# Kernel tuning notes

Measured on AMD Instinct MI355X. Metric: run time of the kernel, lower is better.

The kernel has to match this reference:

```python
import jax, jax.numpy as jnp
import numpy as np

EPS = 1e-5

def _layernorm(x, gamma, beta):
    # normalize over last (channel) axis, per point
    mu = jnp.mean(x, axis=-1, keepdims=True)
    var = jnp.mean(jnp.square(x - mu), axis=-1, keepdims=True)
    return (x - mu) * jax.lax.rsqrt(var + EPS) * gamma + beta

def setup_inputs() -> dict:
    key = jax.random.key(0)
    ks = jax.random.split(key, 12)
    B, N, C, F = 32, 4096, 3, 1024
    points = jax.random.normal(ks[0], (B, N, C), dtype=jnp.float32)
    mask = jax.random.randint(ks[1], (B, 1, N), 0, 2, dtype=jnp.int32)
    s = 0.05
    return {
        "points": points,
        "mask": mask,
        "w1": jax.random.normal(ks[2], (128, C), dtype=jnp.float32) * s,      # conv1 (no bias)
        "g1": jnp.ones((128,), jnp.float32),                                   # norm1 gamma
        "be1": jnp.zeros((128,), jnp.float32),                                 # norm1 beta
        "w2": jax.random.normal(ks[3], (256, 128), dtype=jnp.float32) * s,     # conv2
        "b2": jax.random.normal(ks[4], (256,), dtype=jnp.float32) * s,
        "w3": jax.random.normal(ks[5], (512, 512), dtype=jnp.float32) * s,     # conv3 (no bias)
        "g2": jnp.ones((512,), jnp.float32),                                   # norm2 gamma
        "be2": jnp.zeros((512,), jnp.float32),                                 # norm2 beta
        "w4": jax.random.normal(ks[6], (F, 512), dtype=jnp.float32) * s,       # conv4
        "b4": jax.random.normal(ks[7], (F,), dtype=jnp.float32) * s,
    }

def reference(points, mask, w1, g1, be1, w2, b2, w3, g2, be2, w4, b4):
    # points: [B, N, C]; mask: [B, 1, N]
    vis = (mask[:, 0, :] != 0).astype(points.dtype)[..., None]  # [B, N, 1]
    # conv1 (1x1, no bias) as point-wise matmul
    h0 = jnp.einsum('bnc,kc->bnk', points, w1)                  # [B, N, 128]
    # masked LayerNorm: LN is per-point over channels, so compute densely and zero invisible points
    h1 = _layernorm(h0, g1, be1) * vis
    h2 = jax.nn.relu(h1)
    h3 = jnp.einsum('bnk,ok->bno', h2, w2) + b2                 # [B, N, 256]
    gmax = jnp.max(h3, axis=1, keepdims=True)                   # [B, 1, 256]
    dist = jnp.concatenate([jnp.broadcast_to(gmax, h3.shape), h3], axis=-1)  # [B, N, 512]
    h4 = jnp.einsum('bno,po->bnp', dist, w3)                    # [B, N, 512]
    h5 = _layernorm(h4, g2, be2) * vis
    h6 = jax.nn.relu(h5)
    h7 = jnp.einsum('bnp,fp->bnf', h6, w4) + b4                 # [B, N, F]
    return jnp.max(h7, axis=1)                                  # [B, F]
```

## Files before the change

kernel.cpp:

```cpp
#include <hip/hip_runtime.h>
#include <stdint.h>

#define LN_EPS 1e-5f

static __device__ __forceinline__ unsigned short f2bf_bits(float f) {
  union { float f; unsigned u; } v; v.f = f;
  unsigned r = v.u + 0x7FFFu + ((v.u >> 16) & 1u);
  return (unsigned short)(r >> 16);
}
static __device__ __forceinline__ float bf2f(unsigned short h) {
  union { unsigned u; float f; } v; v.u = ((unsigned)h) << 16;
  return v.f;
}

typedef __bf16 bf16x8 __attribute__((ext_vector_type(8)));
typedef float floatx4 __attribute__((ext_vector_type(4)));

typedef __attribute__((address_space(1))) unsigned int* gas_ptr;
typedef __attribute__((address_space(3))) unsigned int* las_ptr;
static __device__ __forceinline__ void async_cp16(const void* g, void* l) {
  __builtin_amdgcn_global_load_lds((gas_ptr)g, (las_ptr)l, 16, 0, 0);
}

__global__ __launch_bounds__(256) void perm_kernel(
    const int* __restrict__ mask, int* __restrict__ newrow, int* __restrict__ cnt) {
  const int b = blockIdx.x, t = threadIdx.x;
  const int base = b * 4096 + t * 16;
  int v[16]; int s = 0;
#pragma unroll
  for (int i = 0; i < 16; ++i) { v[i] = (mask[base + i] != 0); s += v[i]; }
  const int lane = t & 63, wv = t >> 6;
  int scan = s;
  for (int o = 1; o < 64; o <<= 1) { int x = __shfl_up(scan, o); if (lane >= o) scan += x; }
  __shared__ int wsum[4], woff[4], stotal;
  if (lane == 63) wsum[wv] = scan;
  __syncthreads();
  if (t == 0) { int a = 0; for (int k = 0; k < 4; ++k) { woff[k] = a; a += wsum[k]; } stotal = a; cnt[b] = a; }
  __syncthreads();
  const int excl = scan - s + woff[wv];
  const int total = stotal;
  int run = 0;
#pragma unroll
  for (int i = 0; i < 16; ++i) {
    const int pos = t * 16 + i;
    const int visBefore = excl + run;
    newrow[b * 4096 + pos] = v[i] ? visBefore : total + (pos - visBefore);
    run += v[i];
  }
}

__global__ __launch_bounds__(256) void conv1_ln_kernel(
    const float* __restrict__ points,
    const float* __restrict__ w1, const float* __restrict__ g1,
    const float* __restrict__ be1, unsigned short* __restrict__ h2,
    const int* __restrict__ newrow, const int* __restrict__ cnt,
    const float* __restrict__ w2, const float* __restrict__ b2,
    const float* __restrict__ w3, const float* __restrict__ w4,
    unsigned short* __restrict__ w2b, unsigned short* __restrict__ w4b,
    unsigned short* __restrict__ w23b, float* __restrict__ vecb,
    int* __restrict__ hdr, unsigned short* __restrict__ tl128,
    unsigned short* __restrict__ tl256) {
  if (blockIdx.x >= 32768) {
    const int bb = blockIdx.x - 32768;
    if (bb < 2176) {
      int idx = bb * 256 + threadIdx.x;
      if (idx < 32768) w2b[idx] = f2bf_bits(w2[idx]);
      else w4b[idx - 32768] = f2bf_bits(w4[idx - 32768]);
    } else if (bb < 2176 + 256) {
      const int tid = threadIdx.x;
      const int p = (bb - 2176) * 2 + (tid >> 7);
      const int c = tid & 127;
      const float* w3r = w3 + (size_t)p * 512 + 256;
      float s = 0.f;
      for (int k = 0; k < 256; ++k) s += w3r[k] * w2[k * 128 + c];
      w23b[p * 128 + c] = f2bf_bits(s);
      if (c == 0) {
        float vb = 0.f;
        for (int k = 0; k < 256; ++k) vb += w3r[k] * b2[k];
        vecb[p] = vb;
      }
    } else {
      const int lane = threadIdx.x;
      if (lane < 64) {
        const int c = (lane < 32) ? cnt[lane] : 0;
        const int n128 = (c + 127) >> 7;
        const int n256 = (c + 255) >> 8;
        int s128 = n128, s256 = n256;
        for (int o = 1; o < 64; o <<= 1) {
          int x = __shfl_up(s128, o); if (lane >= o) s128 += x;
          int y = __shfl_up(s256, o); if (lane >= o) s256 += y;
        }
        if (lane == 31) { hdr[0] = s128; hdr[1] = s256; }
        if (lane < 32) {
          const int e128 = s128 - n128, e256 = s256 - n256;
          for (int j = 0; j < n128; ++j) tl128[e128 + j] = (unsigned short)(lane * 32 + j);
          for (int j = 0; j < n256; ++j) tl256[e256 + j] = (unsigned short)(lane * 16 + j);
        }
      }
    }
    return;
  }
  const int lane = threadIdx.x & 63;
  const int wv = threadIdx.x >> 6;
  const size_t p = (size_t)blockIdx.x * 4 + wv;
  const int dest = newrow[p];
  const int cntb = cnt[p >> 12];
  const int ceilv = (cntb + 127) & ~127;
  if (dest >= ceilv) return;
  const bool vis = (dest < cntb);
  const float x0 = points[p * 3 + 0];
  const float x1 = points[p * 3 + 1];
  const float x2 = points[p * 3 + 2];
  const int c0 = lane * 2, c1 = c0 + 1;
  float h00 = w1[c0 * 3] * x0 + w1[c0 * 3 + 1] * x1 + w1[c0 * 3 + 2] * x2;
  float h01 = w1[c1 * 3] * x0 + w1[c1 * 3 + 1] * x1 + w1[c1 * 3 + 2] * x2;
  float s = h00 + h01;
  for (int o = 32; o; o >>= 1) s += __shfl_xor(s, o);
  const float mu = s * (1.f / 128.f);
  const float d0 = h00 - mu, d1 = h01 - mu;
  float q = d0 * d0 + d1 * d1;
  for (int o = 32; o; o >>= 1) q += __shfl_xor(q, o);
  const float rs = rsqrtf(q * (1.f / 128.f) + LN_EPS);
  const float y0 = vis ? fmaxf(d0 * rs * g1[c0] + be1[c0], 0.f) : 0.f;
  const float y1 = vis ? fmaxf(d1 * rs * g1[c1] + be1[c1], 0.f) : 0.f;
  union { unsigned u; unsigned short s2[2]; } pk;
  pk.s2[0] = f2bf_bits(y0);
  pk.s2[1] = f2bf_bits(y1);
  const size_t prow = (p & ~(size_t)4095) + (size_t)dest;
  ((unsigned*)h2)[prow * 64 + lane] = pk.u;
}

__global__ __launch_bounds__(256) void gemm23_fused(
    const unsigned short* __restrict__ A,
    const unsigned short* __restrict__ w2b, const unsigned short* __restrict__ w23b,
    unsigned short* __restrict__ h46, float* __restrict__ pg,
    const float* __restrict__ b2, const float* __restrict__ vecb,
    const int* __restrict__ hdr, const unsigned short* __restrict__ tl128) {
  __shared__ __align__(16) char smA[2][128 * 64];
  __shared__ __align__(16) char smB[2][128 * 64];
  __shared__ float lmax[2][128];

  const int nW = hdr[0] * 6;
  const int cw = (nW + 7) >> 3;
  const int slot = blockIdx.x >> 3;
  const int wI = (blockIdx.x & 7) * cw + slot;
  if (slot >= cw || wI >= nW) return;
  const int t6 = wI / 6;
  const int colTile = wI - t6 * 6;
  const int rowTile = tl128[t6];

  const int tid = threadIdx.x;
  const int lane = tid & 63;
  const int w = tid >> 6;
  const int wm = w >> 1, wn = w & 1;

  const bool isPG = (colTile < 2);
  const int colBase = isPG ? colTile * 128 : (colTile - 2) * 128;
  const size_t rowBase = (size_t)rowTile * 128;
  const unsigned short* Bw = isPG ? w2b : w23b;

  floatx4 acc[4][4];
  const floatx4 zero = {0.f, 0.f, 0.f, 0.f};
#pragma unroll
  for (int i = 0; i < 4; ++i)
#pragma unroll
    for (int j = 0; j < 4; ++j) acc[i][j] = zero;

  const int rSub = lane >> 2;
  const int cb16 = (lane & 3) * 16;
  const size_t Kb = 256;
  const char* gA = (const char*)A + (rowBase + (size_t)(w * 32 + rSub)) * Kb + cb16;
  const char* gB = (const char*)Bw + ((size_t)colBase + (size_t)(w * 32 + rSub)) * Kb + cb16;
  char* lA0 = smA[0] + w * 2048;
  char* lA1 = smA[1] + w * 2048;
  char* lB0 = smB[0] + w * 2048;
  char* lB1 = smB[1] + w * 2048;
  const size_t skip16 = 16 * Kb;

  const int fm = lane & 15, fq = lane >> 4;
  const int fOff = fm * 64 + fq * 16;
  const char* pa0 = smA[0] + wm * 64 * 64 + fOff;
  const char* pa1 = smA[1] + wm * 64 * 64 + fOff;
  const char* pb0 = smB[0] + wn * 64 * 64 + fOff;
  const char* pb1 = smB[1] + wn * 64 * 64 + fOff;

  for (int k0 = 0; k0 < 128; k0 += 64) {
    async_cp16(gA, lA0);
    async_cp16(gA + skip16, lA0 + 1024);
    async_cp16(gA + 64, lA1);
    async_cp16(gA + 64 + skip16, lA1 + 1024);
    async_cp16(gB, lB0);
    async_cp16(gB + skip16, lB0 + 1024);
    async_cp16(gB + 64, lB1);
    async_cp16(gB + 64 + skip16, lB1 + 1024);
    gA += 128; gB += 128;
    __syncthreads();
    bf16x8 af0[4], bg0[4], af1[4], bg1[4];
#pragma unroll
    for (int i = 0; i < 4; ++i) af0[i] = *(const bf16x8*)(pa0 + i * 16 * 64);
#pragma unroll
    for (int j = 0; j < 4; ++j) bg0[j] = *(const bf16x8*)(pb0 + j * 16 * 64);
#pragma unroll
    for (int i = 0; i < 4; ++i)
#pragma unroll
      for (int j = 0; j < 4; ++j)
        acc[i][j] = __builtin_amdgcn_mfma_f32_16x16x32_bf16(af0[i], bg0[j], acc[i][j], 0, 0, 0);
#pragma unroll
    for (int i = 0; i < 4; ++i) af1[i] = *(const bf16x8*)(pa1 + i * 16 * 64);
#pragma unroll
    for (int j = 0; j < 4; ++j) bg1[j] = *(const bf16x8*)(pb1 + j * 16 * 64);
#pragma unroll
    for (int i = 0; i < 4; ++i)
#pragma unroll
      for (int j = 0; j < 4; ++j)
        acc[i][j] = __builtin_amdgcn_mfma_f32_16x16x32_bf16(af1[i], bg1[j], acc[i][j], 0, 0, 0);
    __syncthreads();
  }

  if (isPG) {
    float m4[4] = {-1e30f, -1e30f, -1e30f, -1e30f};
#pragma unroll
    for (int j = 0; j < 4; ++j) {
      const float ex = b2[colBase + wn * 64 + j * 16 + fm];
#pragma unroll
      for (int i = 0; i < 4; ++i)
#pragma unroll
        for (int r = 0; r < 4; ++r) m4[j] = fmaxf(m4[j], acc[i][j][r] + ex);
      m4[j] = fmaxf(m4[j], __shfl_xor(m4[j], 16));
      m4[j] = fmaxf(m4[j], __shfl_xor(m4[j], 32));
    }
    const float sel = (fq == 0) ? m4[0] : (fq == 1) ? m4[1] : (fq == 2) ? m4[2] : m4[3];
    lmax[wm][wn * 64 + fq * 16 + fm] = sel;
    __syncthreads();
    if (tid < 128) {
      const float v = fmaxf(lmax[0][tid], lmax[1][tid]);
      pg[(size_t)rowTile * 256 + colBase + tid] = v;
    }
  } else {
#pragma unroll
    for (int j = 0; j < 4; ++j) {
      const int col = colBase + wn * 64 + j * 16 + fm;
      const float ex = vecb[col];
#pragma unroll
      for (int i = 0; i < 4; ++i) {
        const size_t row0 = rowBase + wm * 64 + i * 16 + fq * 4;
#pragma unroll
        for (int r = 0; r < 4; ++r) {
          h46[(row0 + r) * 512 + col] = f2bf_bits(acc[i][j][r] + ex);
        }
      }
    }
  }
}

#define G4_BAR() __builtin_amdgcn_s_barrier()
#define G4_LGKM0() asm volatile("s_waitcnt lgkmcnt(0)" ::: "memory")
#define G4_LGKM8() asm volatile("s_waitcnt lgkmcnt(8)" ::: "memory")
#define G4_VM2() asm volatile("s_waitcnt vmcnt(2)" ::: "memory")
#define G4_VM0() asm volatile("s_waitcnt vmcnt(0)" ::: "memory")
#define G4_PRIO1() __builtin_amdgcn_s_setprio(1)
#define G4_PRIO0() __builtin_amdgcn_s_setprio(0)

#define G4_STG(bufi, h4, kt) do { \
  const char* _s = (((h4) < 2) ? srcA : srcB) + (size_t)((h4) & 1) * (128 * 1024) + (size_t)(kt) * 128; \
  char* _d = stDst + (bufi) * 65536 + ((h4) >> 1) * 32768 + ((h4) & 1) * 16384; \
  async_cp16(_s, _d); \
  async_cp16(_s + 64 * 1024, _d + 8192); \
} while (0)

#define G4_LDA(bufi, mh) do { \
  const char* _p = rdA + (bufi) * 65536 + (mh) * 8192; \
  af[0][0] = *(const bf16x8*)(_p + c0);        af[0][1] = *(const bf16x8*)(_p + c1); \
  af[1][0] = *(const bf16x8*)(_p + 2048 + c0); af[1][1] = *(const bf16x8*)(_p + 2048 + c1); \
  af[2][0] = *(const bf16x8*)(_p + 4096 + c0); af[2][1] = *(const bf16x8*)(_p + 4096 + c1); \
  af[3][0] = *(const bf16x8*)(_p + 6144 + c0); af[3][1] = *(const bf16x8*)(_p + 6144 + c1); \
} while (0)

#define G4_LDB(bufi, nh, bgx) do { \
  const char* _p = rdB + (bufi) * 65536 + (nh) * 4096; \
  bgx[0][0] = *(const bf16x8*)(_p + c0);        bgx[0][1] = *(const bf16x8*)(_p + c1); \
  bgx[1][0] = *(const bf16x8*)(_p + 2048 + c0); bgx[1][1] = *(const bf16x8*)(_p + 2048 + c1); \
} while (0)

#define G4_QUAD(mh, nh, bgx) do { \
  _Pragma("unroll") \
  for (int _m = 0; _m < 4; ++_m) { \
    _Pragma("unroll") \
    for (int _n = 0; _n < 2; ++_n) { \
      acc[(mh) * 4 + _m][(nh) * 2 + _n] = __builtin_amdgcn_mfma_f32_16x16x32_bf16( \
          af[_m][0], bgx[_n][0], acc[(mh) * 4 + _m][(nh) * 2 + _n], 0, 0, 0); \
      acc[(mh) * 4 + _m][(nh) * 2 + _n] = __builtin_amdgcn_mfma_f32_16x16x32_bf16( \
          af[_m][1], bgx[_n][1], acc[(mh) * 4 + _m][(nh) * 2 + _n], 0, 0, 0); \
    } \
  } \
} while (0)

__global__ __launch_bounds__(512, 2) void gemm4_8ph(
    const unsigned short* __restrict__ A, const unsigned short* __restrict__ Bw,
    float* __restrict__ outp2, const int* __restrict__ hdr,
    const unsigned short* __restrict__ tl256) {
  extern __shared__ char sm[];

  const int nW = hdr[1] * 4;
  const int cw = (nW + 7) >> 3;
  const int slot = blockIdx.x >> 3;
  const int wI = (blockIdx.x & 7) * cw + slot;
  if (slot >= cw || wI >= nW) return;
  const int rowTile = tl256[wI >> 2];
  const int colTile = wI & 3;

  const int tid = threadIdx.x;
  const int lane = tid & 63;
  const int w = tid >> 6;
  const int wm = w >> 2, wn = w & 3;

  const size_t rowBase = (size_t)rowTile * 256;
  const int colBase = colTile * 256;

  const int rr = tid >> 3;
  const int csw = ((tid & 7) ^ (rr & 7)) << 4;
  const char* srcA = (const char*)A + (rowBase + (size_t)rr) * 1024 + csw;
  const char* srcB = (const char*)Bw + ((size_t)colBase + (size_t)rr) * 1024 + csw;
  char* stDst = sm + w * 1024;

  const int fr = lane & 15, fq = lane >> 4;
  const int c0 = (fq * 16) ^ ((lane & 7) << 4);
  const int c1 = ((fq * 16) | 64) ^ ((lane & 7) << 4);
  const char* rdA = sm + (wm * 128 + fr) * 128;
  const char* rdB = sm + 32768 + (wn * 64 + fr) * 128;

  floatx4 acc[8][4];
  const floatx4 zero = {0.f, 0.f, 0.f, 0.f};
#pragma unroll
  for (int i = 0; i < 8; ++i)
#pragma unroll
    for (int j = 0; j < 4; ++j) acc[i][j] = zero;

  bf16x8 af[4][2], bg0[2][2], bg1[2][2];

  G4_STG(0, 0, 0); G4_STG(0, 1, 0); G4_STG(0, 2, 0); G4_STG(0, 3, 0);
  G4_STG(1, 0, 1);
  G4_VM2(); G4_BAR();

  for (int it = 0; it < 3; ++it) {
    const int tO = 2 * it + 1, tE2 = 2 * it + 2, tO2 = 2 * it + 3;
    G4_LDA(0, 0); G4_LDB(0, 0, bg0); G4_STG(1, 1, tO); G4_LGKM8(); G4_BAR(); G4_LGKM0();
    G4_PRIO1(); G4_QUAD(0, 0, bg0); G4_PRIO0(); G4_BAR();
    G4_LDB(0, 1, bg1); G4_STG(1, 2, tO); G4_BAR(); G4_LGKM0();
    G4_PRIO1(); G4_QUAD(0, 1, bg1); G4_PRIO0(); G4_BAR();
    G4_LDA(0, 1); G4_STG(1, 3, tO); G4_BAR(); G4_LGKM0();
    G4_PRIO1(); G4_QUAD(1, 1, bg1); G4_PRIO0(); G4_BAR();
    G4_STG(0, 0, tE2); G4_VM2(); G4_BAR();
    G4_PRIO1(); G4_QUAD(1, 0, bg0); G4_PRIO0(); G4_BAR();
    G4_LDA(1, 0); G4_LDB(1, 0, bg0); G4_STG(0, 1, tE2); G4_LGKM8(); G4_BAR(); G4_LGKM0();
    G4_PRIO1(); G4_QUAD(0, 0, bg0); G4_PRIO0(); G4_BAR();
    G4_LDB(1, 1, bg1); G4_STG(0, 2, tE2); G4_BAR(); G4_LGKM0();
    G4_PRIO1(); G4_QUAD(0, 1, bg1); G4_PRIO0(); G4_BAR();
    G4_LDA(1, 1); G4_STG(0, 3, tE2); G4_BAR(); G4_LGKM0();
    G4_PRIO1(); G4_QUAD(1, 1, bg1); G4_PRIO0(); G4_BAR();
    G4_STG(1, 0, tO2); G4_VM2(); G4_BAR();
    G4_PRIO1(); G4_QUAD(1, 0, bg0); G4_PRIO0(); G4_BAR();
  }

  G4_LDA(0, 0); G4_LDB(0, 0, bg0); G4_STG(1, 1, 7); G4_LGKM8(); G4_BAR(); G4_LGKM0();
  G4_PRIO1(); G4_QUAD(0, 0, bg0); G4_PRIO0(); G4_BAR();
  G4_LDB(0, 1, bg1); G4_STG(1, 2, 7); G4_BAR(); G4_LGKM0();
  G4_PRIO1(); G4_QUAD(0, 1, bg1); G4_PRIO0(); G4_BAR();
  G4_LDA(0, 1); G4_STG(1, 3, 7); G4_BAR(); G4_LGKM0();
  G4_PRIO1(); G4_QUAD(1, 1, bg1); G4_PRIO0(); G4_BAR();
  G4_VM0(); G4_BAR();
  G4_PRIO1(); G4_QUAD(1, 0, bg0); G4_PRIO0(); G4_BAR();
  G4_LDA(1, 0); G4_LDB(1, 0, bg0); G4_BAR(); G4_LGKM0();
  G4_PRIO1(); G4_QUAD(0, 0, bg0); G4_PRIO0(); G4_BAR();
  G4_LDB(1, 1, bg1); G4_BAR(); G4_LGKM0();
  G4_PRIO1(); G4_QUAD(0, 1, bg1); G4_PRIO0(); G4_BAR();
  G4_LDA(1, 1); G4_BAR(); G4_LGKM0();
  G4_PRIO1(); G4_QUAD(1, 1, bg1); G4_PRIO0(); G4_BAR();
  G4_PRIO1(); G4_QUAD(1, 0, bg0); G4_PRIO0(); G4_BAR();

  float* smf = (float*)sm;
  float mv[4];
#pragma unroll
  for (int nj = 0; nj < 4; ++nj) {
    float m = -1e30f;
#pragma unroll
    for (int mi = 0; mi < 8; ++mi)
#pragma unroll
      for (int r = 0; r < 4; ++r) m = fmaxf(m, acc[mi][nj][r]);
    m = fmaxf(m, __shfl_xor(m, 16));
    m = fmaxf(m, __shfl_xor(m, 32));
    mv[nj] = m;
  }
  const float sel = (fq == 0) ? mv[0] : (fq == 1) ? mv[1] : (fq == 2) ? mv[2] : mv[3];
  smf[wm * 256 + wn * 64 + fq * 16 + fr] = sel;
  __syncthreads();
  if (tid < 256) {
    outp2[(size_t)rowTile * 1024 + colBase + tid] = fmaxf(smf[tid], smf[256 + tid]);
  }
}

__global__ __launch_bounds__(256) void gmax_cvec_kernel(
    const float* __restrict__ pg, const float* __restrict__ w3,
    float* __restrict__ cvec, const int* __restrict__ cnt,
    const float* __restrict__ b2) {
  __shared__ float gm[256];
  const int b = blockIdx.x >> 2, quarter = blockIdx.x & 3;
  const int t = threadIdx.x;
  const int c = cnt[b];
  const int nt = (c + 127) >> 7;
  float m = (c < 4096) ? b2[t] : -1e30f;
  for (int s = 0; s < nt; ++s) m = fmaxf(m, pg[((size_t)b * 32 + s) * 256 + t]);
  gm[t] = m;
  __syncthreads();
  const int lane = t & 63, wv = t >> 6;
  const float g0 = gm[lane * 4 + 0];
  const float g1 = gm[lane * 4 + 1];
  const float g2v = gm[lane * 4 + 2];
  const float g3 = gm[lane * 4 + 3];
  for (int pp = 0; pp < 32; ++pp) {
    const int p = quarter * 128 + wv * 32 + pp;
    const float4 wr = *(const float4*)(w3 + (size_t)p * 512 + lane * 4);
    float s = wr.x * g0 + wr.y * g1 + wr.z * g2v + wr.w * g3;
    for (int o = 32; o; o >>= 1) s += __shfl_xor(s, o);
    if (lane == 0) cvec[b * 512 + p] = s;
  }
}

__global__ __launch_bounds__(256) void ln2_kernel(
    unsigned short* __restrict__ h46, const int* __restrict__ cnt,
    const float* __restrict__ cvec,
    const float* __restrict__ g2, const float* __restrict__ be2,
    const int* __restrict__ hdr, const unsigned short* __restrict__ tl256) {
  const int nW = hdr[1] * 64;
  if (blockIdx.x >= nW) return;
  const int rowTile = tl256[blockIdx.x >> 6];
  const int lane = threadIdx.x & 63;
  const int wv = threadIdx.x >> 6;
  const size_t p = (size_t)rowTile * 256 + ((blockIdx.x & 63) * 4 + wv);
  const int b = rowTile >> 4;
  const int cb = cnt[b];
  const int pin = (int)(p & 4095);
  unsigned short* row = h46 + p * 512;
  const int c0 = lane * 8;
  if (pin >= cb) {
    const uint4 z = {0, 0, 0, 0};
    *(uint4*)(row + c0) = z;
    return;
  }
  union { uint4 v; unsigned short s[8]; } in;
  in.v = *(const uint4*)(row + c0);
  float cv[8];
  *(float4*)(cv) = *(const float4*)(cvec + b * 512 + c0);
  *(float4*)(cv + 4) = *(const float4*)(cvec + b * 512 + c0 + 4);
  float f[8];
  float s = 0.f;
#pragma unroll
  for (int k = 0; k < 8; ++k) { f[k] = bf2f(in.s[k]) + cv[k]; s += f[k]; }
  for (int o = 32; o; o >>= 1) s += __shfl_xor(s, o);
  const float mu = s * (1.f / 512.f);
  float q = 0.f;
#pragma unroll
  for (int k = 0; k < 8; ++k) { const float d = f[k] - mu; q += d * d; }
  for (int o = 32; o; o >>= 1) q += __shfl_xor(q, o);
  const float rs = rsqrtf(q * (1.f / 512.f) + LN_EPS);
  union { uint4 v; unsigned short s[8]; } outv;
#pragma unroll
  for (int k = 0; k < 8; ++k) {
    const float y = fmaxf((f[k] - mu) * rs * g2[c0 + k] + be2[c0 + k], 0.f);
    outv.s[k] = f2bf_bits(y);
  }
  *(uint4*)(row + c0) = outv.v;
}

__global__ __launch_bounds__(256) void final_kernel(
    const float* __restrict__ pmax, const float* __restrict__ b4,
    float* __restrict__ out, const int* __restrict__ cnt) {
  const int idx = blockIdx.x * 256 + threadIdx.x;
  const int b = idx >> 10, f = idx & 1023;
  const int c = cnt[b];
  const int nt = (c + 255) >> 8;
  float m = (c < 4096) ? 0.f : -1e30f;
  for (int r = 0; r < nt; ++r) m = fmaxf(m, pmax[((size_t)(b * 16 + r)) * 1024 + f]);
  out[idx] = m + b4[f];
}

extern "C" void kernel_launch(void* const* d_in, const int* in_sizes, int n_in,
                              void* d_out, int out_size, void* d_ws, size_t ws_size,
                              hipStream_t stream) {
  const float* points = (const float*)d_in[0];
  const int* mask = (const int*)d_in[1];
  const float* w1 = (const float*)d_in[2];
  const float* g1 = (const float*)d_in[3];
  const float* be1 = (const float*)d_in[4];
  const float* w2 = (const float*)d_in[5];
  const float* b2 = (const float*)d_in[6];
  const float* w3 = (const float*)d_in[7];
  const float* g2 = (const float*)d_in[8];
  const float* be2 = (const float*)d_in[9];
  const float* w4 = (const float*)d_in[10];
  const float* b4 = (const float*)d_in[11];
  float* out = (float*)d_out;
  char* ws = (char*)d_ws;

  const size_t OFF_H46 = 0;
  const size_t OFF_H2 = 134217728;
  const size_t OFF_W2B = OFF_H2 + 33554432;
  const size_t OFF_W4B = OFF_W2B + 65536;
  const size_t OFF_W23B = OFF_W4B + 1048576;
  const size_t OFF_VECB = OFF_W23B + 131072;
  const size_t OFF_PG = OFF_VECB + 2048;
  const size_t OFF_CVEC = OFF_PG + 1048576;
  const size_t OFF_PMAX = OFF_CVEC + 65536;
  const size_t OFF_CNT = OFF_PMAX + 4194304;
  const size_t OFF_NEWROW = OFF_CNT + 4096;
  const size_t OFF_HDR = OFF_NEWROW + 524288;
  const size_t OFF_TL128 = OFF_HDR + 64;
  const size_t OFF_TL256 = OFF_TL128 + 2048;

  unsigned short* h2 = (unsigned short*)(ws + OFF_H2);
  unsigned short* h46 = (unsigned short*)(ws + OFF_H46);
  unsigned short* w2b = (unsigned short*)(ws + OFF_W2B);
  unsigned short* w4b = (unsigned short*)(ws + OFF_W4B);
  unsigned short* w23b = (unsigned short*)(ws + OFF_W23B);
  float* vecb = (float*)(ws + OFF_VECB);
  float* pg = (float*)(ws + OFF_PG);
  float* cvecp = (float*)(ws + OFF_CVEC);
  float* pmaxp = (float*)(ws + OFF_PMAX);
  int* cntp = (int*)(ws + OFF_CNT);
  int* newrow = (int*)(ws + OFF_NEWROW);
  int* hdr = (int*)(ws + OFF_HDR);
  unsigned short* tl128 = (unsigned short*)(ws + OFF_TL128);
  unsigned short* tl256 = (unsigned short*)(ws + OFF_TL256);

  static bool s_attr_done = false;
  if (!s_attr_done) {
    hipFuncSetAttribute((const void*)gemm4_8ph,
                        hipFuncAttributeMaxDynamicSharedMemorySize, 131072);
    s_attr_done = true;
  }

  perm_kernel<<<32, 256, 0, stream>>>(mask, newrow, cntp);
  conv1_ln_kernel<<<32768 + 2176 + 256 + 1, 256, 0, stream>>>(
      points, w1, g1, be1, h2, newrow, cntp, w2, b2, w3, w4, w2b, w4b, w23b, vecb,
      hdr, tl128, tl256);
  gemm23_fused<<<6144, 256, 0, stream>>>(h2, w2b, w23b, h46, pg, b2, vecb, hdr, tl128);
  gmax_cvec_kernel<<<128, 256, 0, stream>>>(pg, w3, cvecp, cntp, b2);
  ln2_kernel<<<32768, 256, 0, stream>>>(h46, cntp, cvecp, g2, be2, hdr, tl256);
  gemm4_8ph<<<2048, 512, 131072, stream>>>(h46, w4b, pmaxp, hdr, tl256);
  final_kernel<<<128, 256, 0, stream>>>(pmaxp, b4, out, cntp);
}
```

Before: 275.6 us.

## Vectorize conv1 LN stores, stage gemm23 output tile in LDS, static gemm4 tiling

The conv1+LayerNorm kernel now handles 16 points per block, with 16 lanes per point each producing 8 channels. Each lane writes one 16-byte store instead of 4-byte stores, and the block count drops fourfold. The gemm23 h46 epilogue now stages the bf16 tile in shared memory and writes it out as coalesced 16-byte row chunks, replacing scattered 2-byte stores. gemm4 drops the device-built tile list and maps blocks to tiles statically by XCD, exiting early on rows past the per-batch visible count. That removes an indirect lookup but may leave more blocks that launch and exit immediately.

Result: slower. 288.6 us (+4.7%).

```diff
diff --git a/kernel.cpp b/kernel.cpp
--- a/kernel.cpp
+++ b/kernel.cpp
@@ -60,8 +60,8 @@
     unsigned short* __restrict__ w23b, float* __restrict__ vecb,
     int* __restrict__ hdr, unsigned short* __restrict__ tl128,
     unsigned short* __restrict__ tl256) {
-  if (blockIdx.x >= 32768) {
-    const int bb = blockIdx.x - 32768;
+  if (blockIdx.x >= 8192) {
+    const int bb = blockIdx.x - 8192;
     if (bb < 2176) {
       int idx = bb * 256 + threadIdx.x;
       if (idx < 32768) w2b[idx] = f2bf_bits(w2[idx]);
@@ -100,9 +100,9 @@
     }
     return;
   }
-  const int lane = threadIdx.x & 63;
-  const int wv = threadIdx.x >> 6;
-  const size_t p = (size_t)blockIdx.x * 4 + wv;
+  const int tid = threadIdx.x;
+  const int g = tid >> 4, sl = tid & 15;
+  const size_t p = (size_t)blockIdx.x * 16 + g;
   const int dest = newrow[p];
   const int cntb = cnt[p >> 12];
   const int ceilv = (cntb + 127) & ~127;
@@ -111,23 +111,31 @@
   const float x0 = points[p * 3 + 0];
   const float x1 = points[p * 3 + 1];
   const float x2 = points[p * 3 + 2];
-  const int c0 = lane * 2, c1 = c0 + 1;
-  float h00 = w1[c0 * 3] * x0 + w1[c0 * 3 + 1] * x1 + w1[c0 * 3 + 2] * x2;
-  float h01 = w1[c1 * 3] * x0 + w1[c1 * 3 + 1] * x1 + w1[c1 * 3 + 2] * x2;
-  float s = h00 + h01;
-  for (int o = 32; o; o >>= 1) s += __shfl_xor(s, o);
+  float h[8];
+#pragma unroll
+  for (int k = 0; k < 8; ++k) {
+    const int c = sl * 8 + k;
+    h[k] = w1[c * 3] * x0 + w1[c * 3 + 1] * x1 + w1[c * 3 + 2] * x2;
+  }
+  float s = 0.f;
+#pragma unroll
+  for (int k = 0; k < 8; ++k) s += h[k];
+  for (int o = 8; o; o >>= 1) s += __shfl_xor(s, o);
   const float mu = s * (1.f / 128.f);
-  const float d0 = h00 - mu, d1 = h01 - mu;
-  float q = d0 * d0 + d1 * d1;
-  for (int o = 32; o; o >>= 1) q += __shfl_xor(q, o);
+  float d[8]; float q = 0.f;
+#pragma unroll
+  for (int k = 0; k < 8; ++k) { d[k] = h[k] - mu; q += d[k] * d[k]; }
+  for (int o = 8; o; o >>= 1) q += __shfl_xor(q, o);
   const float rs = rsqrtf(q * (1.f / 128.f) + LN_EPS);
-  const float y0 = vis ? fmaxf(d0 * rs * g1[c0] + be1[c0], 0.f) : 0.f;
-  const float y1 = vis ? fmaxf(d1 * rs * g1[c1] + be1[c1], 0.f) : 0.f;
-  union { unsigned u; unsigned short s2[2]; } pk;
-  pk.s2[0] = f2bf_bits(y0);
-  pk.s2[1] = f2bf_bits(y1);
+  union { uint4 v; unsigned short e[8]; } pk;
+#pragma unroll
+  for (int k = 0; k < 8; ++k) {
+    const int c = sl * 8 + k;
+    const float y = vis ? fmaxf(d[k] * rs * g1[c] + be1[c], 0.f) : 0.f;
+    pk.e[k] = f2bf_bits(y);
+  }
   const size_t prow = (p & ~(size_t)4095) + (size_t)dest;
-  ((unsigned*)h2)[prow * 64 + lane] = pk.u;
+  *(uint4*)(h2 + prow * 128 + sl * 8) = pk.v;
 }
 
 __global__ __launch_bounds__(256) void gemm23_fused(
@@ -136,9 +144,12 @@
     unsigned short* __restrict__ h46, float* __restrict__ pg,
     const float* __restrict__ b2, const float* __restrict__ vecb,
     const int* __restrict__ hdr, const unsigned short* __restrict__ tl128) {
-  __shared__ __align__(16) char smA[2][128 * 64];
-  __shared__ __align__(16) char smB[2][128 * 64];
-  __shared__ float lmax[2][128];
+  __shared__ __align__(16) char sraw[33792];
+  char* smA0 = sraw;
+  char* smA1 = sraw + 8192;
+  char* smB0 = sraw + 16384;
+  char* smB1 = sraw + 24576;
+  float* lmax = (float*)(sraw + 32768);
 
   const int nW = hdr[0] * 6;
   const int cw = (nW + 7) >> 3;
@@ -171,18 +182,18 @@
   const size_t Kb = 256;
   const char* gA = (const char*)A + (rowBase + (size_t)(w * 32 + rSub)) * Kb + cb16;
   const char* gB = (const char*)Bw + ((size_t)colBase + (size_t)(w * 32 + rSub)) * Kb + cb16;
-  char* lA0 = smA[0] + w * 2048;
-  char* lA1 = smA[1] + w * 2048;
-  char* lB0 = smB[0] + w * 2048;
-  char* lB1 = smB[1] + w * 2048;
+  char* lA0 = smA0 + w * 2048;
+  char* lA1 = smA1 + w * 2048;
+  char* lB0 = smB0 + w * 2048;
+  char* lB1 = smB1 + w * 2048;
   const size_t skip16 = 16 * Kb;
 
   const int fm = lane & 15, fq = lane >> 4;
   const int fOff = fm * 64 + fq * 16;
-  const char* pa0 = smA[0] + wm * 64 * 64 + fOff;
-  const char* pa1 = smA[1] + wm * 64 * 64 + fOff;
-  const char* pb0 = smB[0] + wn * 64 * 64 + fOff;
-  const char* pb1 = smB[1] + wn * 64 * 64 + fOff;
+  const char* pa0 = smA0 + wm * 64 * 64 + fOff;
+  const char* pa1 = smA1 + wm * 64 * 64 + fOff;
+  const char* pb0 = smB0 + wn * 64 * 64 + fOff;
+  const char* pb1 = smB1 + wn * 64 * 64 + fOff;
 
   for (int k0 = 0; k0 < 128; k0 += 64) {
     async_cp16(gA, lA0);
@@ -230,25 +241,34 @@
       m4[j] = fmaxf(m4[j], __shfl_xor(m4[j], 32));
     }
     const float sel = (fq == 0) ? m4[0] : (fq == 1) ? m4[1] : (fq == 2) ? m4[2] : m4[3];
-    lmax[wm][wn * 64 + fq * 16 + fm] = sel;
+    lmax[wm * 128 + wn * 64 + fq * 16 + fm] = sel;
     __syncthreads();
     if (tid < 128) {
-      const float v = fmaxf(lmax[0][tid], lmax[1][tid]);
+      const float v = fmaxf(lmax[tid], lmax[128 + tid]);
       pg[(size_t)rowTile * 256 + colBase + tid] = v;
     }
   } else {
+    unsigned short* tile = (unsigned short*)sraw;
 #pragma unroll
     for (int j = 0; j < 4; ++j) {
-      const int col = colBase + wn * 64 + j * 16 + fm;
-      const float ex = vecb[col];
+      const int col = wn * 64 + j * 16 + fm;
+      const float ex = vecb[colBase + col];
 #pragma unroll
       for (int i = 0; i < 4; ++i) {
-        const size_t row0 = rowBase + wm * 64 + i * 16 + fq * 4;
-#pragma unroll
-        for (int r = 0; r < 4; ++r) {
-          h46[(row0 + r) * 512 + col] = f2bf_bits(acc[i][j][r] + ex);
-        }
+        const int row0 = wm * 64 + i * 16 + fq * 4;
+#pragma unroll
+        for (int r = 0; r < 4; ++r)
+          tile[(row0 + r) * 128 + col] = f2bf_bits(acc[i][j][r] + ex);
       }
+    }
+    __syncthreads();
+    const int chunk = tid & 15;
+    const int rsub = tid >> 4;
+#pragma unroll
+    for (int qq = 0; qq < 8; ++qq) {
+      const int row = qq * 16 + rsub;
+      const uint4 v = *(const uint4*)(tile + row * 128 + chunk * 8);
+      *(uint4*)(h46 + (rowBase + row) * 512 + colBase + chunk * 8) = v;
     }
   }
 }
@@ -297,25 +317,25 @@
 
 __global__ __launch_bounds__(512, 2) void gemm4_8ph(
     const unsigned short* __restrict__ A, const unsigned short* __restrict__ Bw,
-    float* __restrict__ outp2, const int* __restrict__ hdr,
-    const unsigned short* __restrict__ tl256) {
+    float* __restrict__ outp2, const int* __restrict__ cnt) {
   extern __shared__ char sm[];
 
-  const int nW = hdr[1] * 4;
-  const int cw = (nW + 7) >> 3;
-  const int slot = blockIdx.x >> 3;
-  const int wI = (blockIdx.x & 7) * cw + slot;
-  if (slot >= cw || wI >= nW) return;
-  const int rowTile = tl256[wI >> 2];
-  const int colTile = wI & 3;
+  const int gid = blockIdx.x;
+  const int xcd = gid & 7;
+  const int slot = gid >> 3;
+  const int rowTile = xcd * 64 + (slot >> 2);
+  const int colTile = slot & 3;
+  const size_t rowBase = (size_t)rowTile * 256;
+  const int colBase = colTile * 256;
+
+  const int cntb = cnt[rowBase >> 12];
+  const int rb = (int)(rowBase & 4095);
+  if (rb >= cntb) return;
 
   const int tid = threadIdx.x;
   const int lane = tid & 63;
   const int w = tid >> 6;
   const int wm = w >> 2, wn = w & 3;
-
-  const size_t rowBase = (size_t)rowTile * 256;
-  const int colBase = colTile * 256;
 
   const int rr = tid >> 3;
   const int csw = ((tid & 7) ^ (rr & 7)) << 4;
@@ -540,12 +560,12 @@
   }
 
   perm_kernel<<<32, 256, 0, stream>>>(mask, newrow, cntp);
-  conv1_ln_kernel<<<32768 + 2176 + 256 + 1, 256, 0, stream>>>(
+  conv1_ln_kernel<<<8192 + 2176 + 256 + 1, 256, 0, stream>>>(
       points, w1, g1, be1, h2, newrow, cntp, w2, b2, w3, w4, w2b, w4b, w23b, vecb,
       hdr, tl128, tl256);
   gemm23_fused<<<6144, 256, 0, stream>>>(h2, w2b, w23b, h46, pg, b2, vecb, hdr, tl128);
   gmax_cvec_kernel<<<128, 256, 0, stream>>>(pg, w3, cvecp, cntp, b2);
   ln2_kernel<<<32768, 256, 0, stream>>>(h46, cntp, cvecp, g2, be2, hdr, tl256);
-  gemm4_8ph<<<2048, 512, 131072, stream>>>(h46, w4b, pmaxp, hdr, tl256);
+  gemm4_8ph<<<2048, 512, 131072, stream>>>(h46, w4b, pmaxp, cntp);
   final_kernel<<<128, 256, 0, stream>>>(pmaxp, b4, out, cntp);
 }
```
